# Optimization experiments

Measured on AMD Instinct MI355X. Metric: run time of the kernel, lower is better.

Reference implementation:

```python
import jax, jax.numpy as jnp
import numpy as np

NUM_CLASSES = 2
THRESHOLD = 0.35
NEGPOS_RATIO = 7
VARIANCES = (0.1, 0.2)
B, P, O = 64, 16800, 64  # batch, num_priors, num_objs per image


def point_form(pr):
    # cxcywh -> xyxy
    return jnp.concatenate([pr[:, :2] - pr[:, 2:] / 2, pr[:, :2] + pr[:, 2:] / 2], axis=1)


def jaccard(a, b):
    # a: [A,4] xyxy, b: [Bx,4] xyxy -> IoU [A,Bx]
    lt = jnp.maximum(a[:, None, :2], b[None, :, :2])
    rb = jnp.minimum(a[:, None, 2:], b[None, :, 2:])
    wh = jnp.clip(rb - lt, 0.0)
    inter = wh[..., 0] * wh[..., 1]
    area_a = ((a[:, 2] - a[:, 0]) * (a[:, 3] - a[:, 1]))[:, None]
    area_b = ((b[:, 2] - b[:, 0]) * (b[:, 3] - b[:, 1]))[None, :]
    return inter / (area_a + area_b - inter)


def encode(matched, priors):
    # matched xyxy [P,4], priors cxcywh [P,4]
    g_cxcy = (matched[:, :2] + matched[:, 2:]) / 2 - priors[:, :2]
    g_cxcy = g_cxcy / (VARIANCES[0] * priors[:, 2:])
    g_wh = (matched[:, 2:] - matched[:, :2]) / priors[:, 2:]
    g_wh = jnp.log(g_wh) / VARIANCES[1]
    return jnp.concatenate([g_cxcy, g_wh], axis=1)


def encode_landm(matched, priors):
    # matched [P,10] -> [P,5,2]
    m = matched.reshape(-1, 5, 2)
    g = (m - priors[:, None, :2]) / (VARIANCES[0] * priors[:, None, 2:])
    return g.reshape(-1, 10)


def match_one(truths, labels, landms, priors):
    # truths [O,4], labels [O], landms [O,10]
    overlaps = jaccard(truths, point_form(priors))  # [O,P]
    best_prior_overlap = overlaps.max(axis=1)       # per-gt best IoU
    best_prior_idx = overlaps.argmax(axis=1)
    valid_gt = best_prior_overlap >= 0.2
    best_truth_overlap = overlaps.max(axis=0)       # per-prior best IoU
    best_truth_idx = overlaps.argmax(axis=0)
    # index_fill(2) only for valid gts (best_prior_idx_filter)
    bto = best_truth_overlap.at[best_prior_idx].set(
        jnp.where(valid_gt, 2.0, best_truth_overlap[best_prior_idx]))
    # ensure every gt keeps its best prior
    bti = best_truth_idx.at[best_prior_idx].set(jnp.arange(truths.shape[0]))
    matches = truths[bti]                  # [P,4]
    conf = labels[bti]                     # [P]
    conf = jnp.where(bto < THRESHOLD, 0.0, conf)
    loc = encode(matches, priors)
    landm = encode_landm(landms[bti], priors)
    return loc, conf, landm


def smooth_l1_sum(x, mask):
    ax = jnp.abs(x)
    v = jnp.where(ax < 1.0, 0.5 * ax * ax, ax - 0.5)
    return (v * mask).sum()


def setup_inputs() -> dict:
    key = jax.random.key(0)
    k1, k2, k3, k4, k5, k6, k7, k8 = jax.random.split(key, 8)
    loc_data = jax.random.normal(k1, (B, P, 4), jnp.float32)
    conf_data = jax.random.normal(k2, (B, P, NUM_CLASSES), jnp.float32)
    landm_data = jax.random.normal(k3, (B, P, 10), jnp.float32)
    # priors: cx,cy in (0,1), w,h in (0.02,0.22)
    cxy = jax.random.uniform(k4, (P, 2), jnp.float32)
    wh = jax.random.uniform(k5, (P, 2), jnp.float32) * 0.2 + 0.02
    priors = jnp.concatenate([cxy, wh], axis=1)
    # targets: valid corner boxes + landmarks + label in {1,-1}
    xy1 = jax.random.uniform(k6, (B, O, 2), jnp.float32) * 0.6
    bwh = jax.random.uniform(k7, (B, O, 2), jnp.float32) * 0.3 + 0.05
    boxes = jnp.concatenate([xy1, xy1 + bwh], axis=-1)
    lms = jax.random.uniform(k8, (B, O, 10), jnp.float32)
    lab = jnp.where(jax.random.uniform(jax.random.fold_in(key, 9), (B, O, 1)) < 0.3, -1.0, 1.0)
    targets = jnp.concatenate([boxes, lms, lab], axis=-1)
    return {"loc_data": loc_data, "conf_data": conf_data, "landm_data": landm_data,
            "priors": priors, "targets": targets}


def reference(loc_data, conf_data, landm_data, priors, targets):
    num = loc_data.shape[0]
    num_priors = priors.shape[0]
    truths = targets[:, :, :4]
    landms = targets[:, :, 4:14]
    labels = targets[:, :, -1]
    loc_t, conf_t, landm_t = jax.vmap(match_one, in_axes=(0, 0, 0, None))(
        truths, labels, landms, priors)  # [B,P,4], [B,P], [B,P,10]

    # landmark loss over conf_t > 0
    pos1 = conf_t > 0
    num_pos_landm = pos1.astype(jnp.int32).sum(axis=1, keepdims=True)
    N1 = jnp.maximum(num_pos_landm.sum().astype(jnp.float32), 1.0)
    loss_landm = smooth_l1_sum(landm_data - landm_t, pos1[..., None].astype(landm_data.dtype))

    # localization loss over conf_t != 0 ; conf_t[pos] = 1
    pos = conf_t != 0
    conf_t01 = jnp.where(pos, 1, 0)  # int {0,1}
    loss_l = smooth_l1_sum(loc_data - loc_t, pos[..., None].astype(loc_data.dtype))

    # hard negative mining on per-prior CE loss (global-max log_sum_exp, as in source)
    batch_conf = conf_data.reshape(-1, NUM_CLASSES)
    x_max = batch_conf.max()
    lse = jnp.log(jnp.exp(batch_conf - x_max).sum(axis=1, keepdims=True)) + x_max
    gathered = jnp.take_along_axis(batch_conf, conf_t01.reshape(-1, 1), axis=1)
    loss_c = (lse - gathered).reshape(num, -1)  # [B,P]; positives NOT zeroed (as in source)
    loss_idx = jnp.argsort(-loss_c, axis=1)
    idx_rank = jnp.argsort(loss_idx, axis=1)
    num_pos = pos.astype(jnp.int32).sum(axis=1, keepdims=True)  # [B,1]
    num_neg = jnp.minimum(NEGPOS_RATIO * num_pos, num_priors - 1)
    neg = idx_rank < num_neg  # [B,P]
    neg_pos = pos | neg

    # cross-entropy (sum) over selected pos+neg priors
    logp = jax.nn.log_softmax(conf_data, axis=-1)  # [B,P,C]
    ce = -jnp.take_along_axis(logp, conf_t01[..., None], axis=-1)[..., 0]
    loss_c_final = (ce * neg_pos.astype(ce.dtype)).sum()

    N = jnp.maximum(num_pos.sum().astype(jnp.float32), 1.0)
    return (loss_l / N, loss_c_final / N, loss_landm / N1)
```

## Files before the change

### kernel.cpp

```cpp
#include <hip/hip_runtime.h>
#include <math.h>

#define BN 64
#define PN 16800
#define ON 64
#define THRESH 0.35f
#define NEGPOS 7
#define GX 66
#define NBLK (BN * GX)
#define NBP 1024
#define NCELL 256
#define NCB 66
#define EPSW 0.0009765625f
#define IOUF 0.3499f
#define TAILT 104

struct GAcc {
  unsigned ticket;
  float sl, slm, sc;
  int np, np1;
  unsigned pad0, pad1;
};

__device__ __forceinline__ unsigned f2key(float f) {
  unsigned u = __float_as_uint(f);
  return (u & 0x80000000u) ? ~u : (u | 0x80000000u);
}
__device__ __forceinline__ float key2f(unsigned k) {
  unsigned u = (k & 0x80000000u) ? (k & 0x7FFFFFFFu) : ~k;
  return __uint_as_float(u);
}
__device__ __forceinline__ float sl1(float d) {
  float a = fabsf(d);
  return (a < 1.f) ? 0.5f * a * a : a - 0.5f;
}

__global__ void k_count(const float* __restrict__ priors,
                        unsigned char* __restrict__ pcell,
                        unsigned* __restrict__ bhist,
                        float* __restrict__ gmaxblk,
                        GAcc* __restrict__ gacc) {
  __shared__ unsigned lcnt[NCELL];
  __shared__ float swm[4], swh[4];
  int tid = threadIdx.x;
  int bid = blockIdx.x;
  lcnt[tid] = 0;
  if (bid == 0 && tid < 8) ((unsigned*)gacc)[tid] = 0;
  __syncthreads();
  int p = bid * 256 + tid;
  float mw = 0.f, mh = 0.f;
  if (p < PN) {
    float4 pr = reinterpret_cast<const float4*>(priors)[p];
    int cx = (int)(pr.x * 16.f); cx = cx < 0 ? 0 : (cx > 15 ? 15 : cx);
    int cy = (int)(pr.y * 16.f); cy = cy < 0 ? 0 : (cy > 15 ? 15 : cy);
    int cell = cy * 16 + cx;
    pcell[p] = (unsigned char)cell;
    atomicAdd(&lcnt[cell], 1u);
    mw = pr.z * 0.5f;
    mh = pr.w * 0.5f;
  }
#pragma unroll
  for (int off = 32; off; off >>= 1) {
    mw = fmaxf(mw, __shfl_xor(mw, off));
    mh = fmaxf(mh, __shfl_xor(mh, off));
  }
  if ((tid & 63) == 0) { swm[tid >> 6] = mw; swh[tid >> 6] = mh; }
  __syncthreads();
  if (tid == 0) {
    gmaxblk[bid * 2] = fmaxf(fmaxf(swm[0], swm[1]), fmaxf(swm[2], swm[3]));
    gmaxblk[bid * 2 + 1] = fmaxf(fmaxf(swh[0], swh[1]), fmaxf(swh[2], swh[3]));
  }
  bhist[bid * NCELL + tid] = lcnt[tid];
}

__global__ void k_scatter(const float* __restrict__ priors,
                          const float* __restrict__ targets,
                          const unsigned char* __restrict__ pcell,
                          const unsigned* __restrict__ bhist,
                          const float* __restrict__ gmaxblk,
                          unsigned* __restrict__ gmax,
                          float4* __restrict__ sbox,
                          int* __restrict__ sorig,
                          int* __restrict__ cellOff,
                          unsigned long long* __restrict__ tmask) {
  int bid = blockIdx.x;
  int tid = threadIdx.x;
  if (bid < NCB) {
    __shared__ unsigned tmp[NCELL];
    __shared__ unsigned sbase[NCELL];
    __shared__ unsigned lcnt[NCELL];
    unsigned tot = 0, mybase = 0;
#pragma unroll 4
    for (int b2 = 0; b2 < NCB; b2++) {
      unsigned h = bhist[b2 * NCELL + tid];
      if (b2 < bid) mybase += h;
      tot += h;
    }
    tmp[tid] = tot;
    lcnt[tid] = 0;
    __syncthreads();
    for (int off = 1; off < NCELL; off <<= 1) {
      unsigned v = (tid >= off) ? tmp[tid - off] : 0u;
      __syncthreads();
      tmp[tid] += v;
      __syncthreads();
    }
    unsigned excl = tmp[tid] - tot;
    sbase[tid] = excl + mybase;
    if (bid == 0) {
      cellOff[tid] = (int)excl;
      if (tid == 0) {
        cellOff[NCELL] = PN;
        float MW = 0.f, MH = 0.f;
        for (int i = 0; i < NCB; i++) {
          MW = fmaxf(MW, gmaxblk[2 * i]);
          MH = fmaxf(MH, gmaxblk[2 * i + 1]);
        }
        gmax[0] = __float_as_uint(MW);
        gmax[1] = __float_as_uint(MH);
      }
    }
    __syncthreads();
    int p = bid * 256 + tid;
    if (p < PN) {
      int cell = pcell[p];
      unsigned lrank = atomicAdd(&lcnt[cell], 1u);
      int slot = (int)(sbase[cell] + lrank);
      float4 pr = reinterpret_cast<const float4*>(priors)[p];
      float px1 = pr.x - pr.z * 0.5f, py1 = pr.y - pr.w * 0.5f;
      float px2 = pr.x + pr.z * 0.5f, py2 = pr.y + pr.w * 0.5f;
      sbox[slot] = make_float4(px1, py1, px2, py2);
      sorig[slot] = p;
    }
  } else {
    int b = bid - NCB;
    __shared__ float4 tb[ON];
    if (tid < ON) {
      const float* tg = &targets[((long)b * ON + tid) * 15];
      tb[tid] = make_float4(tg[0], tg[1], tg[2], tg[3]);
    }
    __syncthreads();
    float MW = 0.f, MH = 0.f;
    for (int i = 0; i < NCB; i++) {
      MW = fmaxf(MW, gmaxblk[2 * i]);
      MH = fmaxf(MH, gmaxblk[2 * i + 1]);
    }
    int cx = tid & 15, cy = tid >> 4;
    float cxl = (float)cx * 0.0625f, cxh = (float)(cx + 1) * 0.0625f;
    float cyl = (float)cy * 0.0625f, cyh = (float)(cy + 1) * 0.0625f;
    float pmaxa = 4.f * MW * MH;
    unsigned long long m = 0ull;
    for (int t = 0; t < ON; t++) {
      float4 a = tb[t];
      float wt = a.z - a.x, ht = a.w - a.y;
      float at = wt * ht;
      float need = IOUF * at;
      float wmin = need / fminf(ht, 2.f * MH);
      float hmin = need / fminf(wt, 2.f * MW);
      float wx0 = a.x + wmin - MW - EPSW, wx1 = a.z - wmin + MW + EPSW;
      float wy0 = a.y + hmin - MH - EPSW, wy1 = a.w - hmin + MH + EPSW;
      bool ok = (pmaxa >= need) &&
                (cxh > wx0) && (cxl < wx1) &&
                (cyh > wy0) && (cyl < wy1);
      if (ok) m |= (1ull << t);
    }
    tmask[b * NCELL + tid] = m;
  }
}

__global__ void k_bp(const float* __restrict__ targets,
                     const float4* __restrict__ sbox,
                     const int* __restrict__ sorig,
                     const int* __restrict__ cellOff,
                     const unsigned* __restrict__ gmax,
                     unsigned long long* __restrict__ bpp) {
  int bid = blockIdx.x;
  int tid = threadIdx.x;
  int lane = tid & 63, wv = tid >> 6;
  int b = bid >> 4;
  int t = ((bid & 15) << 2) + wv;
  const float* tg = &targets[((long)b * ON + t) * 15];
  float ax1 = tg[0], ay1 = tg[1], ax2 = tg[2], ay2 = tg[3];
  float aa = (ax2 - ax1) * (ay2 - ay1);
  float MW = __uint_as_float(gmax[0]), MH = __uint_as_float(gmax[1]);
  int xlo = (int)floorf((ax1 - MW - EPSW) * 16.f); xlo = xlo < 0 ? 0 : (xlo > 15 ? 15 : xlo);
  int xhi = (int)floorf((ax2 + MW + EPSW) * 16.f); xhi = xhi < 0 ? 0 : (xhi > 15 ? 15 : xhi);
  int ylo = (int)floorf((ay1 - MH - EPSW) * 16.f); ylo = ylo < 0 ? 0 : (ylo > 15 ? 15 : ylo);
  int yhi = (int)floorf((ay2 + MH + EPSW) * 16.f); yhi = yhi < 0 ? 0 : (yhi > 15 ? 15 : yhi);
  float bi = 0.f, bu = 1.f; int bp = 0;
  for (int cy = ylo; cy <= yhi; cy++) {
    int s0 = cellOff[cy * 16 + xlo];
    int s1 = cellOff[cy * 16 + xhi + 1];
    for (int s = s0 + lane; s < s1; s += 64) {
      float4 pr = sbox[s];
      int op = sorig[s];
      float ab2 = (pr.z - pr.x) * (pr.w - pr.y);
      float lx = fmaxf(ax1, pr.x), ly = fmaxf(ay1, pr.y);
      float rx = fminf(ax2, pr.z), ry = fminf(ay2, pr.w);
      float w = fmaxf(rx - lx, 0.f), h = fmaxf(ry - ly, 0.f);
      float inter = w * h;
      float uni = aa + ab2 - inter;
      float A = inter * bu, C = bi * uni;
      if (A > C || (A == C && op < bp)) { bi = inter; bu = uni; bp = op; }
    }
  }
#pragma unroll
  for (int off = 1; off < 64; off <<= 1) {
    float oi = __shfl_xor(bi, off), ou = __shfl_xor(bu, off);
    int op = __shfl_xor(bp, off);
    float A = oi * bu, C = bi * ou;
    if (A > C || (A == C && op < bp)) { bi = oi; bu = ou; bp = op; }
  }
  if (lane == 0) {
    float q = bi / bu;
    bpp[(long)b * ON + t] = ((unsigned long long)f2key(q) << 32) | (unsigned)(~bp);
  }
}

__global__ void k_encode(const float* __restrict__ loc_data,
                         const float* __restrict__ conf_data,
                         const float* __restrict__ landm_data,
                         const float* __restrict__ priors,
                         const float* __restrict__ targets,
                         const unsigned char* __restrict__ pcell,
                         const unsigned long long* __restrict__ tmask,
                         const unsigned long long* __restrict__ bpp,
                         float* __restrict__ lossc, unsigned char* __restrict__ posf,
                         float* __restrict__ part_l, float* __restrict__ part_lm,
                         int* __restrict__ np_part, int* __restrict__ np1_part) {
  int b = blockIdx.y;
  int p = blockIdx.x * 256 + threadIdx.x;
  int bid = b * GX + blockIdx.x;
  __shared__ float4 tgs4[ON * 15 / 4];
  __shared__ float4 tb[ON];
  __shared__ float ta[ON];
  __shared__ unsigned long long smask[NCELL];
  __shared__ int ovr[256];
  float* tgs = (float*)tgs4;
  if (threadIdx.x < ON * 15 / 4)
    tgs4[threadIdx.x] = reinterpret_cast<const float4*>(targets + (long)b * ON * 15)[threadIdx.x];
  smask[threadIdx.x] = tmask[b * NCELL + threadIdx.x];
  if (threadIdx.x < ON) {
    const float* tg = &targets[((long)b * ON + threadIdx.x) * 15];
    float4 bx = make_float4(tg[0], tg[1], tg[2], tg[3]);
    tb[threadIdx.x] = bx;
    ta[threadIdx.x] = (bx.z - bx.x) * (bx.w - bx.y);
  }
  ovr[threadIdx.x] = -1;
  __syncthreads();
  if (threadIdx.x < ON) {
    int t = threadIdx.x;
    unsigned long long best = bpp[(long)b * ON + t];
    float q = key2f((unsigned)(best >> 32));
    int qp = (int)(~(unsigned)best);
    int s0 = blockIdx.x * 256;
    if (qp >= s0 && qp < s0 + 256) {
      int valid = (q >= 0.2f) ? 1 : 0;
      atomicMax(&ovr[qp - s0], (t << 1) | valid);
    }
  }
  __syncthreads();

  float sum_l = 0.f, sum_lm = 0.f;
  int cp = 0, cp1 = 0;
  if (p < PN) {
    float4 pr = reinterpret_cast<const float4*>(priors)[p];
    float px1 = pr.x - pr.z * 0.5f, py1 = pr.y - pr.w * 0.5f;
    float px2 = pr.x + pr.z * 0.5f, py2 = pr.y + pr.w * 0.5f;
    float ab2 = (px2 - px1) * (py2 - py1);
    unsigned long long m = smask[pcell[p]];
    float bi = 0.f, bu = 1.f; int t = 0;
    while (m) {
      int t0 = __builtin_ctzll(m); m &= m - 1;
      float4 a0 = tb[t0]; float aa0 = ta[t0];
      if (m) {
        int t1 = __builtin_ctzll(m); m &= m - 1;
        float4 a1 = tb[t1]; float aa1 = ta[t1];
        float lx0 = fmaxf(a0.x, px1), ly0 = fmaxf(a0.y, py1);
        float rx0 = fminf(a0.z, px2), ry0 = fminf(a0.w, py2);
        float w0 = fmaxf(rx0 - lx0, 0.f), h0 = fmaxf(ry0 - ly0, 0.f);
        float in0 = w0 * h0, un0 = aa0 + ab2 - in0;
        float lx1 = fmaxf(a1.x, px1), ly1 = fmaxf(a1.y, py1);
        float rx1 = fminf(a1.z, px2), ry1 = fminf(a1.w, py2);
        float w1 = fmaxf(rx1 - lx1, 0.f), h1 = fmaxf(ry1 - ly1, 0.f);
        float in1 = w1 * h1, un1 = aa1 + ab2 - in1;
        if (in0 * bu > bi * un0) { bi = in0; bu = un0; t = t0; }
        if (in1 * bu > bi * un1) { bi = in1; bu = un1; t = t1; }
      } else {
        float lx = fmaxf(a0.x, px1), ly = fmaxf(a0.y, py1);
        float rx = fminf(a0.z, px2), ry = fminf(a0.w, py2);
        float w2 = fmaxf(rx - lx, 0.f), h2 = fmaxf(ry - ly, 0.f);
        float inter = w2 * h2;
        float uni = aa0 + ab2 - inter;
        if (inter * bu > bi * uni) { bi = inter; bu = uni; t = t0; }
      }
    }
    bool pos = (bi / bu) >= THRESH;
    int o = ovr[threadIdx.x];
    if (o >= 0) { t = o >> 1; if (o & 1) pos = true; }
    const float* tg = &tgs[t * 15];
    float label = tg[14];
    bool pos1 = pos && (label > 0.f);
    if (pos) {
      float rz = 1.0f / pr.z, rw = 1.0f / pr.w;
      float m0 = tg[0], m1 = tg[1], m2 = tg[2], m3 = tg[3];
      float g0 = ((m0 + m2) * 0.5f - pr.x) * rz * 10.f;
      float g1 = ((m1 + m3) * 0.5f - pr.y) * rw * 10.f;
      float g2 = __logf((m2 - m0) * rz) * 5.f;
      float g3 = __logf((m3 - m1) * rw) * 5.f;
      const float* ld = &loc_data[((long)b * PN + p) * 4];
      sum_l = sl1(ld[0] - g0) + sl1(ld[1] - g1) + sl1(ld[2] - g2) + sl1(ld[3] - g3);
      cp = 1;
      if (pos1) {
        const float* lm = &landm_data[((long)b * PN + p) * 10];
#pragma unroll
        for (int i = 0; i < 5; i++) {
          float gx = (tg[4 + 2 * i] - pr.x) * rz * 10.f;
          float gy = (tg[5 + 2 * i] - pr.y) * rw * 10.f;
          sum_lm += sl1(lm[2 * i] - gx) + sl1(lm[2 * i + 1] - gy);
        }
        cp1 = 1;
      }
    }
    float2 c2 = reinterpret_cast<const float2*>(conf_data)[(long)b * PN + p];
    float mx = fmaxf(c2.x, c2.y);
    float lse = mx + __logf(__expf(c2.x - mx) + __expf(c2.y - mx));
    lossc[b * PN + p] = lse - (pos ? c2.y : c2.x);
    posf[b * PN + p] = pos ? 1 : 0;
  }
  for (int off = 32; off; off >>= 1) {
    sum_l += __shfl_down(sum_l, off);
    sum_lm += __shfl_down(sum_lm, off);
    cp += __shfl_down(cp, off);
    cp1 += __shfl_down(cp1, off);
  }
  __shared__ float sl4[4], slm4[4];
  __shared__ int sp4[4], sp14[4];
  int w = threadIdx.x >> 6;
  if ((threadIdx.x & 63) == 0) { sl4[w] = sum_l; slm4[w] = sum_lm; sp4[w] = cp; sp14[w] = cp1; }
  __syncthreads();
  if (threadIdx.x == 0) {
    part_l[bid] = sl4[0] + sl4[1] + sl4[2] + sl4[3];
    part_lm[bid] = slm4[0] + slm4[1] + slm4[2] + slm4[3];
    np_part[bid] = sp4[0] + sp4[1] + sp4[2] + sp4[3];
    np1_part[bid] = sp14[0] + sp14[1] + sp14[2] + sp14[3];
  }
}

__global__ void __launch_bounds__(1024) k_select(const float* __restrict__ lossc,
                                                 const unsigned char* __restrict__ posf,
                                                 const int* __restrict__ np_part,
                                                 const int* __restrict__ np1_part,
                                                 const float* __restrict__ part_l,
                                                 const float* __restrict__ part_lm,
                                                 GAcc* __restrict__ gacc,
                                                 float* __restrict__ out) {
  int b = blockIdx.x;
  int tid = threadIdx.x;
  int lane = tid & 63;
  int wv = tid >> 6;
  __shared__ int s_np, s_rnp1;
  __shared__ float s_rsl, s_rslm;
  __shared__ unsigned s_lo, s_hi, s_cg, s_totp;
  __shared__ unsigned fcnt[16];
  __shared__ unsigned wsc[16];
  __shared__ float wsum[16];
  const float* row = &lossc[(long)b * PN];
  const unsigned char* prow = &posf[(long)b * PN];

  if (tid == 0) {
    s_np = 0; s_rnp1 = 0; s_rsl = 0.f; s_rslm = 0.f;
    s_lo = 0u; s_hi = 0xFFFFFFFFu;
  }
  __syncthreads();
  if (tid < GX) {
    atomicAdd(&s_np, np_part[b * GX + tid]);
    atomicAdd(&s_rsl, part_l[b * GX + tid]);
    atomicAdd(&s_rslm, part_lm[b * GX + tid]);
    atomicAdd(&s_rnp1, np1_part[b * GX + tid]);
  }

  const float4* rf4 = reinterpret_cast<const float4*>(row);
  const uint4* pw4 = reinterpret_cast<const uint4*>(prow);
  bool hasTail = tid < TAILT;
  float vm[16];
  float vt[4];
  {
    float4 L0 = rf4[tid * 4], L1 = rf4[tid * 4 + 1], L2 = rf4[tid * 4 + 2], L3 = rf4[tid * 4 + 3];
    vm[0] = L0.x; vm[1] = L0.y; vm[2] = L0.z; vm[3] = L0.w;
    vm[4] = L1.x; vm[5] = L1.y; vm[6] = L1.z; vm[7] = L1.w;
    vm[8] = L2.x; vm[9] = L2.y; vm[10] = L2.z; vm[11] = L2.w;
    vm[12] = L3.x; vm[13] = L3.y; vm[14] = L3.z; vm[15] = L3.w;
  }
  unsigned pmask = 0;
  {
    uint4 W = pw4[tid];
    unsigned w0 = W.x, w1 = W.y, w2 = W.z, w3 = W.w;
#pragma unroll
    for (int j = 0; j < 4; j++) {
      pmask |= ((w0 >> (8 * j)) & 1u) << j;
      pmask |= ((w1 >> (8 * j)) & 1u) << (4 + j);
      pmask |= ((w2 >> (8 * j)) & 1u) << (8 + j);
      pmask |= ((w3 >> (8 * j)) & 1u) << (12 + j);
    }
  }
  unsigned tmask = 0;
  if (hasTail) {
    float4 Lt = rf4[4096 + tid];
    vt[0] = Lt.x; vt[1] = Lt.y; vt[2] = Lt.z; vt[3] = Lt.w;
    unsigned Wt = reinterpret_cast<const unsigned*>(prow)[4096 + tid];
#pragma unroll
    for (int j = 0; j < 4; j++) tmask |= ((Wt >> (8 * j)) & 1u) << j;
  } else {
    vt[0] = vt[1] = vt[2] = vt[3] = -1.f;
  }
  unsigned km[16], kt4[4];
#pragma unroll
  for (int j = 0; j < 16; j++) km[j] = f2key(vm[j]);
#pragma unroll
  for (int j = 0; j < 4; j++) kt4[j] = f2key(vt[j]);
  __syncthreads();
  int np = s_np;
  int k = NEGPOS * np;
  if (k > PN - 1) k = PN - 1;
  bool haveNeg = (k > 0);

  unsigned T = 0, Rsel = 0;
  if (haveNeg) {
    for (int it = 0; it < 32; it++) {
      unsigned lo = s_lo, hi = s_hi;
      unsigned mid = lo + ((hi - lo) >> 1) + ((hi - lo) & 1u);
      unsigned c = 0;
#pragma unroll
      for (int j = 0; j < 16; j++) c += (km[j] >= mid) ? 1u : 0u;
      if (hasTail) {
#pragma unroll
        for (int j = 0; j < 4; j++) c += (kt4[j] >= mid) ? 1u : 0u;
      }
#pragma unroll
      for (int o = 32; o; o >>= 1) c += (unsigned)__shfl_down((int)c, o);
      if (lane == 0) fcnt[wv] = c;
      __syncthreads();
      if (tid == 0) {
        unsigned tot = 0;
        for (int i = 0; i < 16; i++) tot += fcnt[i];
        if (tot >= (unsigned)k) s_lo = mid; else s_hi = mid - 1;
      }
      __syncthreads();
      if (s_lo >= s_hi) break;
    }
    T = s_lo;
    unsigned c = 0;
#pragma unroll
    for (int j = 0; j < 16; j++) c += (km[j] > T) ? 1u : 0u;
    if (hasTail) {
#pragma unroll
      for (int j = 0; j < 4; j++) c += (kt4[j] > T) ? 1u : 0u;
    }
#pragma unroll
    for (int o = 32; o; o >>= 1) c += (unsigned)__shfl_down((int)c, o);
    if (lane == 0) fcnt[wv] = c;
    __syncthreads();
    if (tid == 0) {
      unsigned tot = 0;
      for (int i = 0; i < 16; i++) tot += fcnt[i];
      s_cg = tot;
    }
    __syncthreads();
    Rsel = (unsigned)k - s_cg;
  }

  unsigned mc = 0, tc = 0;
  if (haveNeg) {
#pragma unroll
    for (int j = 0; j < 16; j++) mc += (km[j] == T) ? 1u : 0u;
    if (hasTail) {
#pragma unroll
      for (int j = 0; j < 4; j++) tc += (kt4[j] == T) ? 1u : 0u;
    }
  }
  unsigned packed = mc | (tc << 16);
  unsigned inc = packed;
#pragma unroll
  for (int o = 1; o < 64; o <<= 1) {
    unsigned u = (unsigned)__shfl_up((int)inc, o);
    if (lane >= o) inc += u;
  }
  if (lane == 63) wsc[wv] = inc;
  __syncthreads();
  if (tid == 0) {
    unsigned run = 0;
    for (int i = 0; i < 16; i++) { unsigned t2 = wsc[i]; wsc[i] = run; run += t2; }
    s_totp = run;
  }
  __syncthreads();
  unsigned excl = wsc[wv] + inc - packed;
  unsigned mb = excl & 0xFFFFu;
  unsigned tb2 = (s_totp & 0xFFFFu) + (excl >> 16);

  float acc = 0.f;
  unsigned cm = 0;
#pragma unroll
  for (int j = 0; j < 16; j++) {
    float v2 = vm[j];
    bool pos = (pmask >> j) & 1u;
    if (pos) acc += v2;
    if (haveNeg) {
      if (km[j] > T) { if (!pos) acc += v2; }
      else if (km[j] == T) {
        unsigned r2 = mb + cm; cm++;
        if (!pos && r2 < Rsel) acc += v2;
      }
    }
  }
  if (hasTail) {
    unsigned ct = 0;
#pragma unroll
    for (int j = 0; j < 4; j++) {
      float v2 = vt[j];
      bool pos = (tmask >> j) & 1u;
      if (pos) acc += v2;
      if (haveNeg) {
        if (kt4[j] > T) { if (!pos) acc += v2; }
        else if (kt4[j] == T) {
          unsigned r2 = tb2 + ct; ct++;
          if (!pos && r2 < Rsel) acc += v2;
        }
      }
    }
  }
#pragma unroll
  for (int o = 32; o; o >>= 1) acc += __shfl_down(acc, o);
  if (lane == 0) wsum[wv] = acc;
  __syncthreads();

  if (tid == 0) {
    float tot = 0.f;
    for (int i = 0; i < 16; i++) tot += wsum[i];
    atomicAdd(&gacc->sc, tot);
    atomicAdd(&gacc->sl, s_rsl);
    atomicAdd(&gacc->slm, s_rslm);
    atomicAdd(&gacc->np, np);
    atomicAdd(&gacc->np1, s_rnp1);
  }
  __threadfence();
  __shared__ int lastF;
  if (tid == 0) lastF = (atomicAdd(&gacc->ticket, 1u) == (unsigned)(BN - 1)) ? 1 : 0;
  __syncthreads();
  if (lastF && tid == 0) {
    __threadfence();
    float sl = atomicAdd(&gacc->sl, 0.f);
    float slm = atomicAdd(&gacc->slm, 0.f);
    float sc = atomicAdd(&gacc->sc, 0.f);
    int tnp = atomicAdd(&gacc->np, 0);
    int tnp1 = atomicAdd(&gacc->np1, 0);
    float N = fmaxf((float)tnp, 1.f);
    float N1 = fmaxf((float)tnp1, 1.f);
    out[0] = sl / N;
    out[1] = sc / N;
    out[2] = slm / N1;
  }
}

extern "C" void kernel_launch(void* const* d_in, const int* in_sizes, int n_in,
                              void* d_out, int out_size, void* d_ws, size_t ws_size,
                              hipStream_t stream) {
  const float* loc_data = (const float*)d_in[0];
  const float* conf_data = (const float*)d_in[1];
  const float* landm_data = (const float*)d_in[2];
  const float* priors = (const float*)d_in[3];
  const float* targets = (const float*)d_in[4];
  float* out = (float*)d_out;

  char* ws = (char*)d_ws;
  size_t off = 0;
  float* lossc = (float*)(ws + off); off += (size_t)BN * PN * 4;
  unsigned char* posf = (unsigned char*)(ws + off); off += (size_t)BN * PN;
  off = (off + 15) & ~(size_t)15;
  unsigned long long* bpp = (unsigned long long*)(ws + off); off += (size_t)BN * ON * 8;
  float* part_l = (float*)(ws + off); off += NBLK * 4;
  float* part_lm = (float*)(ws + off); off += NBLK * 4;
  int* np_part = (int*)(ws + off); off += NBLK * 4;
  int* np1_part = (int*)(ws + off); off += NBLK * 4;
  float4* sbox = (float4*)(ws + off); off += (size_t)PN * 16;
  int* sorig = (int*)(ws + off); off += (size_t)PN * 4;
  unsigned char* pcell = (unsigned char*)(ws + off); off += (size_t)PN;
  off = (off + 15) & ~(size_t)15;
  int* cellOff = (int*)(ws + off); off += 260 * 4;
  unsigned long long* tmask = (unsigned long long*)(ws + off); off += (size_t)BN * NCELL * 8;
  off = (off + 15) & ~(size_t)15;
  unsigned* bhist = (unsigned*)(ws + off); off += (size_t)NCB * NCELL * 4;
  float* gmaxblk = (float*)(ws + off); off += (size_t)NCB * 2 * 4;
  unsigned* gmax = (unsigned*)(ws + off); off += 16;
  GAcc* gacc = (GAcc*)(ws + off); off += sizeof(GAcc);

  k_count<<<NCB, 256, 0, stream>>>(priors, pcell, bhist, gmaxblk, gacc);
  k_scatter<<<NCB + BN, 256, 0, stream>>>(priors, targets, pcell, bhist, gmaxblk, gmax,
                                          sbox, sorig, cellOff, tmask);
  k_bp<<<NBP, 256, 0, stream>>>(targets, sbox, sorig, cellOff, gmax, bpp);
  dim3 gbp(GX, BN);
  k_encode<<<gbp, 256, 0, stream>>>(loc_data, conf_data, landm_data, priors, targets,
                                    pcell, tmask, bpp, lossc, posf,
                                    part_l, part_lm, np_part, np1_part);
  k_select<<<BN, 1024, 0, stream>>>(lossc, posf, np_part, np1_part, part_l, part_lm,
                                    gacc, out);
}
```

Measured before the change: 224.5 us.

## Use 16-way radix search on 64-bit keys and replace atomic finalization with separate kernel

The k_select threshold search moves from a 32-step binary search on 32-bit keys to a 16-way split search on 64-bit keys. Each key packs the loss with the inverted index, which makes every key unique and removes the tie-handling prefix scan. This cuts the number of block-wide synchronisation rounds per row. The atomic ticket-based global reduction is replaced by per-row partial writes and a tiny k_final kernel. The cost is more comparisons per round, 64-bit register pressure, and an extra kernel launch.

New measurement: 276.3 us. 1.23x slower.

```diff
diff --git a/kernel.cpp b/kernel.cpp
--- a/kernel.cpp
+++ b/kernel.cpp
@@ -15,13 +15,6 @@
 #define IOUF 0.3499f
 #define TAILT 104
 
-struct GAcc {
-  unsigned ticket;
-  float sl, slm, sc;
-  int np, np1;
-  unsigned pad0, pad1;
-};
-
 __device__ __forceinline__ unsigned f2key(float f) {
   unsigned u = __float_as_uint(f);
   return (u & 0x80000000u) ? ~u : (u | 0x80000000u);
@@ -38,14 +31,12 @@
 __global__ void k_count(const float* __restrict__ priors,
                         unsigned char* __restrict__ pcell,
                         unsigned* __restrict__ bhist,
-                        float* __restrict__ gmaxblk,
-                        GAcc* __restrict__ gacc) {
+                        float* __restrict__ gmaxblk) {
   __shared__ unsigned lcnt[NCELL];
   __shared__ float swm[4], swh[4];
   int tid = threadIdx.x;
   int bid = blockIdx.x;
   lcnt[tid] = 0;
-  if (bid == 0 && tid < 8) ((unsigned*)gacc)[tid] = 0;
   __syncthreads();
   int p = bid * 256 + tid;
   float mw = 0.f, mh = 0.f;
@@ -353,24 +344,22 @@
                                                  const int* __restrict__ np1_part,
                                                  const float* __restrict__ part_l,
                                                  const float* __restrict__ part_lm,
-                                                 GAcc* __restrict__ gacc,
-                                                 float* __restrict__ out) {
+                                                 float* __restrict__ rout) {
   int b = blockIdx.x;
   int tid = threadIdx.x;
   int lane = tid & 63;
   int wv = tid >> 6;
   __shared__ int s_np, s_rnp1;
   __shared__ float s_rsl, s_rslm;
-  __shared__ unsigned s_lo, s_hi, s_cg, s_totp;
-  __shared__ unsigned fcnt[16];
-  __shared__ unsigned wsc[16];
+  __shared__ unsigned long long s_lo, s_hi;
+  __shared__ unsigned fpack[16][8];
   __shared__ float wsum[16];
   const float* row = &lossc[(long)b * PN];
   const unsigned char* prow = &posf[(long)b * PN];
 
   if (tid == 0) {
     s_np = 0; s_rnp1 = 0; s_rsl = 0.f; s_rslm = 0.f;
-    s_lo = 0u; s_hi = 0xFFFFFFFFu;
+    s_lo = 0ull; s_hi = 0xFFFFFFFFFFFFFFFFull;
   }
   __syncthreads();
   if (tid < GX) {
@@ -381,181 +370,153 @@
   }
 
   const float4* rf4 = reinterpret_cast<const float4*>(row);
-  const uint4* pw4 = reinterpret_cast<const uint4*>(prow);
+  const unsigned* pw = reinterpret_cast<const unsigned*>(prow);
+  float4 v4[4];
+  unsigned pm[4];
+#pragma unroll
+  for (int c = 0; c < 4; c++) {
+    v4[c] = rf4[c * 1024 + tid];
+    pm[c] = pw[c * 1024 + tid];
+  }
   bool hasTail = tid < TAILT;
-  float vm[16];
-  float vt[4];
+  float4 vt4;
+  unsigned pmt = 0;
+  if (hasTail) {
+    vt4 = rf4[4096 + tid];
+    pmt = pw[4096 + tid];
+  } else {
+    vt4 = make_float4(-1.f, -1.f, -1.f, -1.f);
+  }
+  unsigned long long K[20];
+#pragma unroll
+  for (int c = 0; c < 4; c++) {
+    const float* vf = (const float*)&v4[c];
+    int e0 = 4 * (c * 1024 + tid);
+#pragma unroll
+    for (int f = 0; f < 4; f++)
+      K[c * 4 + f] = ((unsigned long long)f2key(vf[f]) << 32) | (unsigned)(~(e0 + f));
+  }
   {
-    float4 L0 = rf4[tid * 4], L1 = rf4[tid * 4 + 1], L2 = rf4[tid * 4 + 2], L3 = rf4[tid * 4 + 3];
-    vm[0] = L0.x; vm[1] = L0.y; vm[2] = L0.z; vm[3] = L0.w;
-    vm[4] = L1.x; vm[5] = L1.y; vm[6] = L1.z; vm[7] = L1.w;
-    vm[8] = L2.x; vm[9] = L2.y; vm[10] = L2.z; vm[11] = L2.w;
-    vm[12] = L3.x; vm[13] = L3.y; vm[14] = L3.z; vm[15] = L3.w;
-  }
-  unsigned pmask = 0;
-  {
-    uint4 W = pw4[tid];
-    unsigned w0 = W.x, w1 = W.y, w2 = W.z, w3 = W.w;
-#pragma unroll
-    for (int j = 0; j < 4; j++) {
-      pmask |= ((w0 >> (8 * j)) & 1u) << j;
-      pmask |= ((w1 >> (8 * j)) & 1u) << (4 + j);
-      pmask |= ((w2 >> (8 * j)) & 1u) << (8 + j);
-      pmask |= ((w3 >> (8 * j)) & 1u) << (12 + j);
-    }
-  }
-  unsigned tmask = 0;
-  if (hasTail) {
-    float4 Lt = rf4[4096 + tid];
-    vt[0] = Lt.x; vt[1] = Lt.y; vt[2] = Lt.z; vt[3] = Lt.w;
-    unsigned Wt = reinterpret_cast<const unsigned*>(prow)[4096 + tid];
-#pragma unroll
-    for (int j = 0; j < 4; j++) tmask |= ((Wt >> (8 * j)) & 1u) << j;
-  } else {
-    vt[0] = vt[1] = vt[2] = vt[3] = -1.f;
-  }
-  unsigned km[16], kt4[4];
-#pragma unroll
-  for (int j = 0; j < 16; j++) km[j] = f2key(vm[j]);
-#pragma unroll
-  for (int j = 0; j < 4; j++) kt4[j] = f2key(vt[j]);
+    const float* vf = (const float*)&vt4;
+    int e0 = 4 * (4096 + tid);
+#pragma unroll
+    for (int f = 0; f < 4; f++)
+      K[16 + f] = ((unsigned long long)f2key(vf[f]) << 32) | (unsigned)(~(e0 + f));
+  }
   __syncthreads();
   int np = s_np;
   int k = NEGPOS * np;
   if (k > PN - 1) k = PN - 1;
   bool haveNeg = (k > 0);
 
-  unsigned T = 0, Rsel = 0;
+  unsigned long long T = 0ull;
   if (haveNeg) {
-    for (int it = 0; it < 32; it++) {
-      unsigned lo = s_lo, hi = s_hi;
-      unsigned mid = lo + ((hi - lo) >> 1) + ((hi - lo) & 1u);
-      unsigned c = 0;
-#pragma unroll
-      for (int j = 0; j < 16; j++) c += (km[j] >= mid) ? 1u : 0u;
-      if (hasTail) {
-#pragma unroll
-        for (int j = 0; j < 4; j++) c += (kt4[j] >= mid) ? 1u : 0u;
-      }
-#pragma unroll
-      for (int o = 32; o; o >>= 1) c += (unsigned)__shfl_down((int)c, o);
-      if (lane == 0) fcnt[wv] = c;
+    for (int it = 0; it < 20; ++it) {
+      unsigned long long lo = s_lo, hi = s_hi;
+      if (lo >= hi) break;
+      unsigned long long step = (hi - lo) / 16ull + 1ull;
+      unsigned cnt[15];
+#pragma unroll
+      for (int j = 0; j < 15; j++) {
+        unsigned long long pj = lo + (unsigned long long)(j + 1) * step;
+        unsigned c = 0;
+#pragma unroll
+        for (int e = 0; e < 20; e++) c += (K[e] >= pj) ? 1u : 0u;
+        cnt[j] = c;
+      }
+      unsigned pk[8];
+#pragma unroll
+      for (int i = 0; i < 7; i++) pk[i] = cnt[2 * i] | (cnt[2 * i + 1] << 16);
+      pk[7] = cnt[14];
+#pragma unroll
+      for (int i = 0; i < 8; i++) {
+#pragma unroll
+        for (int o = 32; o; o >>= 1) pk[i] += (unsigned)__shfl_down((int)pk[i], o);
+      }
+      if (lane == 0) {
+#pragma unroll
+        for (int i = 0; i < 8; i++) fpack[wv][i] = pk[i];
+      }
       __syncthreads();
-      if (tid == 0) {
-        unsigned tot = 0;
-        for (int i = 0; i < 16; i++) tot += fcnt[i];
-        if (tot >= (unsigned)k) s_lo = mid; else s_hi = mid - 1;
+      if (wv == 0) {
+        bool q = false;
+        if (lane == 0) q = true;
+        else if (lane <= 15) {
+          int cj = lane - 1;
+          int idx = cj >> 1;
+          int sh = (cj & 1) * 16;
+          unsigned tot = 0;
+          for (int w2 = 0; w2 < 16; w2++) tot += (fpack[w2][idx] >> sh) & 0xFFFFu;
+          q = tot >= (unsigned)k;
+        }
+        unsigned long long mk = __ballot(q) & 0xFFFFull;
+        if (lane == 0) {
+          int j = 63 - __clzll(mk);
+          unsigned long long nlo = lo + (unsigned long long)j * step;
+          unsigned long long nhi = (j < 15) ? (lo + (unsigned long long)(j + 1) * step - 1ull) : hi;
+          s_lo = nlo; s_hi = nhi;
+        }
       }
       __syncthreads();
-      if (s_lo >= s_hi) break;
     }
     T = s_lo;
-    unsigned c = 0;
-#pragma unroll
-    for (int j = 0; j < 16; j++) c += (km[j] > T) ? 1u : 0u;
-    if (hasTail) {
-#pragma unroll
-      for (int j = 0; j < 4; j++) c += (kt4[j] > T) ? 1u : 0u;
-    }
-#pragma unroll
-    for (int o = 32; o; o >>= 1) c += (unsigned)__shfl_down((int)c, o);
-    if (lane == 0) fcnt[wv] = c;
-    __syncthreads();
-    if (tid == 0) {
-      unsigned tot = 0;
-      for (int i = 0; i < 16; i++) tot += fcnt[i];
-      s_cg = tot;
-    }
-    __syncthreads();
-    Rsel = (unsigned)k - s_cg;
-  }
-
-  unsigned mc = 0, tc = 0;
-  if (haveNeg) {
-#pragma unroll
-    for (int j = 0; j < 16; j++) mc += (km[j] == T) ? 1u : 0u;
-    if (hasTail) {
-#pragma unroll
-      for (int j = 0; j < 4; j++) tc += (kt4[j] == T) ? 1u : 0u;
-    }
-  }
-  unsigned packed = mc | (tc << 16);
-  unsigned inc = packed;
-#pragma unroll
-  for (int o = 1; o < 64; o <<= 1) {
-    unsigned u = (unsigned)__shfl_up((int)inc, o);
-    if (lane >= o) inc += u;
-  }
-  if (lane == 63) wsc[wv] = inc;
-  __syncthreads();
-  if (tid == 0) {
-    unsigned run = 0;
-    for (int i = 0; i < 16; i++) { unsigned t2 = wsc[i]; wsc[i] = run; run += t2; }
-    s_totp = run;
-  }
-  __syncthreads();
-  unsigned excl = wsc[wv] + inc - packed;
-  unsigned mb = excl & 0xFFFFu;
-  unsigned tb2 = (s_totp & 0xFFFFu) + (excl >> 16);
+  }
 
   float acc = 0.f;
-  unsigned cm = 0;
-#pragma unroll
-  for (int j = 0; j < 16; j++) {
-    float v2 = vm[j];
-    bool pos = (pmask >> j) & 1u;
-    if (pos) acc += v2;
-    if (haveNeg) {
-      if (km[j] > T) { if (!pos) acc += v2; }
-      else if (km[j] == T) {
-        unsigned r2 = mb + cm; cm++;
-        if (!pos && r2 < Rsel) acc += v2;
-      }
-    }
-  }
-  if (hasTail) {
-    unsigned ct = 0;
-#pragma unroll
-    for (int j = 0; j < 4; j++) {
-      float v2 = vt[j];
-      bool pos = (tmask >> j) & 1u;
-      if (pos) acc += v2;
-      if (haveNeg) {
-        if (kt4[j] > T) { if (!pos) acc += v2; }
-        else if (kt4[j] == T) {
-          unsigned r2 = tb2 + ct; ct++;
-          if (!pos && r2 < Rsel) acc += v2;
-        }
-      }
+#pragma unroll
+  for (int c = 0; c < 4; c++) {
+    const float* vf = (const float*)&v4[c];
+#pragma unroll
+    for (int f = 0; f < 4; f++) {
+      float v = vf[f];
+      bool pos = (pm[c] >> (8 * f)) & 1u;
+      if (pos) acc += v;
+      else if (haveNeg && K[c * 4 + f] >= T) acc += v;
+    }
+  }
+  {
+    const float* vf = (const float*)&vt4;
+#pragma unroll
+    for (int f = 0; f < 4; f++) {
+      float v = vf[f];
+      bool pos = (pmt >> (8 * f)) & 1u;
+      if (pos) acc += v;
+      else if (haveNeg && K[16 + f] >= T) acc += v;
     }
   }
 #pragma unroll
   for (int o = 32; o; o >>= 1) acc += __shfl_down(acc, o);
   if (lane == 0) wsum[wv] = acc;
   __syncthreads();
-
   if (tid == 0) {
     float tot = 0.f;
     for (int i = 0; i < 16; i++) tot += wsum[i];
-    atomicAdd(&gacc->sc, tot);
-    atomicAdd(&gacc->sl, s_rsl);
-    atomicAdd(&gacc->slm, s_rslm);
-    atomicAdd(&gacc->np, np);
-    atomicAdd(&gacc->np1, s_rnp1);
-  }
-  __threadfence();
-  __shared__ int lastF;
-  if (tid == 0) lastF = (atomicAdd(&gacc->ticket, 1u) == (unsigned)(BN - 1)) ? 1 : 0;
-  __syncthreads();
-  if (lastF && tid == 0) {
-    __threadfence();
-    float sl = atomicAdd(&gacc->sl, 0.f);
-    float slm = atomicAdd(&gacc->slm, 0.f);
-    float sc = atomicAdd(&gacc->sc, 0.f);
-    int tnp = atomicAdd(&gacc->np, 0);
-    int tnp1 = atomicAdd(&gacc->np1, 0);
-    float N = fmaxf((float)tnp, 1.f);
-    float N1 = fmaxf((float)tnp1, 1.f);
+    rout[b * 8 + 0] = tot;
+    rout[b * 8 + 1] = s_rsl;
+    rout[b * 8 + 2] = s_rslm;
+    ((int*)rout)[b * 8 + 3] = np;
+    ((int*)rout)[b * 8 + 4] = s_rnp1;
+  }
+}
+
+__global__ void k_final(const float* __restrict__ rout, float* __restrict__ out) {
+  int tid = threadIdx.x;
+  float sc = rout[tid * 8 + 0];
+  float sl = rout[tid * 8 + 1];
+  float slm = rout[tid * 8 + 2];
+  int np = ((const int*)rout)[tid * 8 + 3];
+  int np1 = ((const int*)rout)[tid * 8 + 4];
+#pragma unroll
+  for (int o = 32; o; o >>= 1) {
+    sc += __shfl_down(sc, o);
+    sl += __shfl_down(sl, o);
+    slm += __shfl_down(slm, o);
+    np += __shfl_down(np, o);
+    np1 += __shfl_down(np1, o);
+  }
+  if (tid == 0) {
+    float N = fmaxf((float)np, 1.f);
+    float N1 = fmaxf((float)np1, 1.f);
     out[0] = sl / N;
     out[1] = sc / N;
     out[2] = slm / N1;
@@ -592,9 +553,9 @@
   unsigned* bhist = (unsigned*)(ws + off); off += (size_t)NCB * NCELL * 4;
   float* gmaxblk = (float*)(ws + off); off += (size_t)NCB * 2 * 4;
   unsigned* gmax = (unsigned*)(ws + off); off += 16;
-  GAcc* gacc = (GAcc*)(ws + off); off += sizeof(GAcc);
-
-  k_count<<<NCB, 256, 0, stream>>>(priors, pcell, bhist, gmaxblk, gacc);
+  float* rout = (float*)(ws + off); off += (size_t)BN * 8 * 4;
+
+  k_count<<<NCB, 256, 0, stream>>>(priors, pcell, bhist, gmaxblk);
   k_scatter<<<NCB + BN, 256, 0, stream>>>(priors, targets, pcell, bhist, gmaxblk, gmax,
                                           sbox, sorig, cellOff, tmask);
   k_bp<<<NBP, 256, 0, stream>>>(targets, sbox, sorig, cellOff, gmax, bpp);
@@ -603,5 +564,6 @@
                                     pcell, tmask, bpp, lossc, posf,
                                     part_l, part_lm, np_part, np1_part);
   k_select<<<BN, 1024, 0, stream>>>(lossc, posf, np_part, np1_part, part_l, part_lm,
-                                    gacc, out);
-}
+                                    rout);
+  k_final<<<1, 64, 0, stream>>>(rout, out);
+}
```
